# Optimization experiments

Measured on AMD Instinct MI355X. Metric: run time of the kernel, lower is better.

Reference implementation:

```python
import jax, jax.numpy as jnp
import numpy as np

N_NODES = 50000
N_EDGES = 640000
IN_CH, HID, OUT_CH = 128, 256, 3


def setup_inputs() -> dict:
    key = jax.random.key(0)
    ks = jax.random.split(key, 6)
    x = jax.random.normal(ks[0], (N_NODES, IN_CH), dtype=jnp.float32)
    edge_index = jax.random.randint(ks[1], (2, N_EDGES), 0, N_NODES, dtype=jnp.int64)
    # Glorot-ish scaling for weights
    Wl0 = jax.random.normal(ks[2], (IN_CH, HID), dtype=jnp.float32) / np.sqrt(IN_CH)
    bl0 = jnp.zeros((HID,), dtype=jnp.float32)
    Wr0 = jax.random.normal(ks[3], (IN_CH, HID), dtype=jnp.float32) / np.sqrt(IN_CH)
    Wl1 = jax.random.normal(ks[4], (HID, OUT_CH), dtype=jnp.float32) / np.sqrt(HID)
    bl1 = jnp.zeros((OUT_CH,), dtype=jnp.float32)
    Wr1 = jax.random.normal(ks[5], (HID, OUT_CH), dtype=jnp.float32) / np.sqrt(HID)
    return {"x": x, "edge_index": edge_index, "Wl0": Wl0, "bl0": bl0, "Wr0": Wr0,
            "Wl1": Wl1, "bl1": bl1, "Wr1": Wr1}


def _sage_conv(x, src, dst, Wl, bl, Wr, num_nodes):
    # mean aggregation of source features into destination nodes
    msg_sum = jax.ops.segment_sum(x[src], dst, num_segments=num_nodes)  # [N, d_in]
    deg = jax.ops.segment_sum(jnp.ones((src.shape[0],), x.dtype), dst, num_segments=num_nodes)
    mean = msg_sum / jnp.maximum(deg, 1.0)[:, None]
    # PyG SAGEConv: lin_l(aggr) + lin_r(x_self); lin_l carries the bias
    return mean @ Wl + bl + x @ Wr


def reference(x, edge_index, Wl0, bl0, Wr0, Wl1, bl1, Wr1):
    src, dst = edge_index[0], edge_index[1]
    h = _sage_conv(x, src, dst, Wl0, bl0, Wr0, N_NODES)
    h = jax.nn.relu(h)
    # dropout is identity in eval mode (training=False)
    return _sage_conv(h, src, dst, Wl1, bl1, Wr1, N_NODES)
```

## Files before the change

### kernel.cpp

```cpp
#include <hip/hip_runtime.h>

#define NN 50000
#define NNP 50048
#define NE 640000
#define IC 128
#define HC 256
#define OC 3
#define PAD 64

#define TOBF16_BLOCKS (NN * IC / 8 / 256)
#define WPACK_BLOCKS  32
#define DEGZ_BLOCKS   ((NN * 16 / 4 + 255) / 256)

typedef __attribute__((ext_vector_type(8))) short short8;
typedef __attribute__((ext_vector_type(4))) float f32x4;

__device__ __forceinline__ unsigned short f2bf(float f) {
    unsigned int u = __float_as_uint(f);
    unsigned int r = u + 0x7FFFu + ((u >> 16) & 1u);
    return (unsigned short)(r >> 16);
}
__device__ __forceinline__ float bflo(unsigned int v) { return __uint_as_float(v << 16); }
__device__ __forceinline__ float bfhi(unsigned int v) { return __uint_as_float(v & 0xffff0000u); }

__global__ __launch_bounds__(256) void k_prep(const float* __restrict__ x,
                                              const float* __restrict__ Wl0,
                                              const float* __restrict__ Wr0,
                                              unsigned short* __restrict__ Ab,
                                              unsigned short* __restrict__ Bp,
                                              int* __restrict__ degi) {
    int b = blockIdx.x;
    int t = threadIdx.x;
    if (b < TOBF16_BLOCKS) {
        int i = b * 256 + t;
        int n = i >> 4;
        int c = (i & 15) * 8;
        float4 v0 = ((const float4*)x)[i * 2];
        float4 v1 = ((const float4*)x)[i * 2 + 1];
        ushort4 o0, o1;
        o0.x = f2bf(v0.x); o0.y = f2bf(v0.y); o0.z = f2bf(v0.z); o0.w = f2bf(v0.w);
        o1.x = f2bf(v1.x); o1.y = f2bf(v1.y); o1.z = f2bf(v1.z); o1.w = f2bf(v1.w);
        *(ushort4*)&Ab[(size_t)n * 256 + 128 + c] = o0;
        *(ushort4*)&Ab[(size_t)n * 256 + 128 + c + 4] = o1;
    } else if (b < TOBF16_BLOCKS + WPACK_BLOCKS) {
        int tt = (b - TOBF16_BLOCKS) * 256 + t;
        int l = tt & 63;
        int nt = (tt >> 6) & 15;
        int kt = tt >> 10;
        int n = nt * 16 + (l & 15);
        int kbase = kt * 32 + (l >> 4) * 8;
        unsigned short o[8];
        #pragma unroll
        for (int e = 0; e < 8; ++e) {
            int k = kbase + e;
            float w = (k < IC) ? Wl0[k * HC + n] : Wr0[(k - IC) * HC + n];
            o[e] = f2bf(w);
        }
        #pragma unroll
        for (int e = 0; e < 8; ++e) Bp[(size_t)tt * 8 + e] = o[e];
    } else {
        int idx = (b - TOBF16_BLOCKS - WPACK_BLOCKS) * 256 + t;
        if (idx < NN * 16 / 4) ((uint4*)degi)[idx] = make_uint4(0u, 0u, 0u, 0u);
    }
}

__global__ __launch_bounds__(256) void k_build(const int* __restrict__ ei,
                                               int* __restrict__ degi,
                                               unsigned short* __restrict__ csrp) {
    int e = blockIdx.x * blockDim.x + threadIdx.x;
    if (e >= NE) return;
    int src = ei[e];
    int dst = ei[NE + e];
    int rank = atomicAdd(&degi[dst << 4], 1);
    if (rank < PAD) csrp[dst * PAD + rank] = (unsigned short)src;
}

__global__ __launch_bounds__(256) void k_agg(const int* __restrict__ degi,
                                             const unsigned short* __restrict__ csrp,
                                             unsigned short* __restrict__ Ab) {
    int wid = (blockIdx.x * blockDim.x + threadIdx.x) >> 6;
    int lane = threadIdx.x & 63;
    if (wid >= NN) return;
    int deg = min(degi[wid << 4], PAD);
    int beg = wid * PAD;
    int sg = lane >> 3;
    int s  = lane & 7;
    const uint4* base = (const uint4*)Ab;

    float a[16];
    #pragma unroll
    for (int i = 0; i < 16; ++i) a[i] = 0.f;

    for (int j = sg; j < deg; j += 8) {
        int src = csrp[beg + j];
        uint4 v0 = base[(size_t)src * 32 + 16 + s];
        uint4 v1 = base[(size_t)src * 32 + 24 + s];
        a[0] += bflo(v0.x); a[1] += bfhi(v0.x);
        a[2] += bflo(v0.y); a[3] += bfhi(v0.y);
        a[4] += bflo(v0.z); a[5] += bfhi(v0.z);
        a[6] += bflo(v0.w); a[7] += bfhi(v0.w);
        a[8]  += bflo(v1.x); a[9]  += bfhi(v1.x);
        a[10] += bflo(v1.y); a[11] += bfhi(v1.y);
        a[12] += bflo(v1.z); a[13] += bfhi(v1.z);
        a[14] += bflo(v1.w); a[15] += bfhi(v1.w);
    }
    #pragma unroll
    for (int m = 8; m <= 32; m <<= 1)
        #pragma unroll
        for (int i = 0; i < 16; ++i) a[i] += __shfl_xor(a[i], m);

    if (sg == 0) {
        float inv = 1.0f / fmaxf((float)deg, 1.0f);
        uint4 o0, o1;
        o0.x = ((unsigned int)f2bf(a[1] * inv) << 16) | f2bf(a[0] * inv);
        o0.y = ((unsigned int)f2bf(a[3] * inv) << 16) | f2bf(a[2] * inv);
        o0.z = ((unsigned int)f2bf(a[5] * inv) << 16) | f2bf(a[4] * inv);
        o0.w = ((unsigned int)f2bf(a[7] * inv) << 16) | f2bf(a[6] * inv);
        o1.x = ((unsigned int)f2bf(a[9]  * inv) << 16) | f2bf(a[8]  * inv);
        o1.y = ((unsigned int)f2bf(a[11] * inv) << 16) | f2bf(a[10] * inv);
        o1.z = ((unsigned int)f2bf(a[13] * inv) << 16) | f2bf(a[12] * inv);
        o1.w = ((unsigned int)f2bf(a[15] * inv) << 16) | f2bf(a[14] * inv);
        ((uint4*)Ab)[(size_t)wid * 32 + s] = o0;
        ((uint4*)Ab)[(size_t)wid * 32 + 8 + s] = o1;
    }
}

__global__ __launch_bounds__(256, 4) void k_gemm(const unsigned short* __restrict__ Ab,
                                                 const unsigned short* __restrict__ Bp,
                                                 const float* __restrict__ bl0,
                                                 const float* __restrict__ Wl1,
                                                 const float* __restrict__ Wr1,
                                                 float* __restrict__ g,
                                                 float* __restrict__ r) {
    __shared__ float4 Bs[2048];
    __shared__ float wl1s[HC][3];
    __shared__ float wr1s[HC][3];
    __shared__ float bls[HC];

    int t = threadIdx.x;
    for (int i = t; i < HC * 3; i += 256) {
        wl1s[i / 3][i % 3] = Wl1[i];
        wr1s[i / 3][i % 3] = Wr1[i];
    }
    for (int i = t; i < HC; i += 256) bls[i] = bl0[i];

    int w = t >> 6, l = t & 63;
    int n0 = blockIdx.x * 64 + w * 16;

    f32x4 acc[16];
    #pragma unroll
    for (int i = 0; i < 16; ++i) acc[i] = (f32x4){0.f, 0.f, 0.f, 0.f};

    const short8* A8 = (const short8*)Ab + ((size_t)(n0 + (l & 15)) * 32 + (l >> 4));

    for (int q = 0; q < 4; ++q) {
        short8 af0 = A8[(q * 2 + 0) * 4];
        short8 af1 = A8[(q * 2 + 1) * 4];
        __syncthreads();
        const float4* gsrc = (const float4*)(Bp + (size_t)q * 16384) + (w * 64 + l);
        float4* lbase = Bs + w * 64;
        #pragma unroll
        for (int i = 0; i < 8; ++i) {
            __builtin_amdgcn_global_load_lds(
                (const __attribute__((address_space(1))) void*)(gsrc + i * 256),
                (__attribute__((address_space(3))) void*)(lbase + i * 256),
                16, 0, 0);
        }
        __syncthreads();
        const short8* B8 = (const short8*)Bs + l;
        #pragma unroll
        for (int nt = 0; nt < 16; ++nt) {
            short8 bf = B8[nt * 64];
            acc[nt] = __builtin_amdgcn_mfma_f32_16x16x32_bf16(af0, bf, acc[nt], 0, 0, 0);
        }
        B8 = (const short8*)Bs + (1024 + l);
        #pragma unroll
        for (int nt = 0; nt < 16; ++nt) {
            short8 bf = B8[nt * 64];
            acc[nt] = __builtin_amdgcn_mfma_f32_16x16x32_bf16(af1, bf, acc[nt], 0, 0, 0);
        }
    }

    float pl[4][3] = {{0.f}}, pr[4][3] = {{0.f}};
    #pragma unroll
    for (int nt = 0; nt < 16; ++nt) {
        int col = nt * 16 + (l & 15);
        float b = bls[col];
        #pragma unroll
        for (int e = 0; e < 4; ++e) {
            float h = fmaxf(acc[nt][e] + b, 0.0f);
            #pragma unroll
            for (int j = 0; j < 3; ++j) {
                pl[e][j] = fmaf(h, wl1s[col][j], pl[e][j]);
                pr[e][j] = fmaf(h, wr1s[col][j], pr[e][j]);
            }
        }
    }
    #pragma unroll
    for (int m = 1; m <= 8; m <<= 1) {
        #pragma unroll
        for (int e = 0; e < 4; ++e)
            #pragma unroll
            for (int j = 0; j < 3; ++j) {
                pl[e][j] += __shfl_xor(pl[e][j], m);
                pr[e][j] += __shfl_xor(pr[e][j], m);
            }
    }
    if ((l & 15) == 0) {
        #pragma unroll
        for (int e = 0; e < 4; ++e) {
            int node = n0 + (l >> 4) * 4 + e;
            if (node < NN) {
                #pragma unroll
                for (int j = 0; j < 3; ++j) {
                    g[node * 3 + j] = pl[e][j];
                    r[node * 3 + j] = pr[e][j];
                }
            }
        }
    }
}

__global__ __launch_bounds__(256) void k_out(const int* __restrict__ degi,
                                             const unsigned short* __restrict__ csrp,
                                             const float* __restrict__ g,
                                             const float* __restrict__ r,
                                             const float* __restrict__ bl1,
                                             float* __restrict__ out) {
    int tid = blockIdx.x * 256 + threadIdx.x;
    int n = tid >> 3;
    int sl = tid & 7;
    if (n >= NN) return;
    int deg = min(degi[n << 4], PAD);
    int beg = n * PAD;
    float s0 = 0.f, s1 = 0.f, s2 = 0.f;
    for (int j = sl; j < deg; j += 8) {
        int src = csrp[beg + j];
        s0 += g[src * 3 + 0];
        s1 += g[src * 3 + 1];
        s2 += g[src * 3 + 2];
    }
    #pragma unroll
    for (int m = 1; m < 8; m <<= 1) {
        s0 += __shfl_xor(s0, m);
        s1 += __shfl_xor(s1, m);
        s2 += __shfl_xor(s2, m);
    }
    if (sl == 0) {
        float inv = 1.0f / fmaxf((float)deg, 1.0f);
        out[n * 3 + 0] = s0 * inv + bl1[0] + r[n * 3 + 0];
        out[n * 3 + 1] = s1 * inv + bl1[1] + r[n * 3 + 1];
        out[n * 3 + 2] = s2 * inv + bl1[2] + r[n * 3 + 2];
    }
}

extern "C" void kernel_launch(void* const* d_in, const int* in_sizes, int n_in,
                              void* d_out, int out_size, void* d_ws, size_t ws_size,
                              hipStream_t stream) {
    const float* x   = (const float*)d_in[0];
    const int*   ei  = (const int*)d_in[1];
    const float* Wl0 = (const float*)d_in[2];
    const float* bl0 = (const float*)d_in[3];
    const float* Wr0 = (const float*)d_in[4];
    const float* Wl1 = (const float*)d_in[5];
    const float* bl1 = (const float*)d_in[6];
    const float* Wr1 = (const float*)d_in[7];
    float* out = (float*)d_out;

    char* ws = (char*)d_ws;
    int*            degi = (int*)(ws);
    unsigned short* csrp = (unsigned short*)(ws + 3200064);
    unsigned short* Ab   = (unsigned short*)(ws + 9600064);
    unsigned short* Bp   = (unsigned short*)(ws + 35224640);
    float*          g    = (float*)(ws + 35355712);
    float*          r    = (float*)(ws + 35955776);

    k_prep <<<TOBF16_BLOCKS + WPACK_BLOCKS + DEGZ_BLOCKS, 256, 0, stream>>>(x, Wl0, Wr0, Ab, Bp, degi);
    k_build<<<(NE + 255) / 256, 256, 0, stream>>>(ei, degi, csrp);
    k_agg  <<<(NN * 64 + 255) / 256, 256, 0, stream>>>(degi, csrp, Ab);
    k_gemm <<<(NN + 63) / 64, 256, 0, stream>>>(Ab, Bp, bl0, Wl1, Wr1, g, r);
    k_out  <<<(NN * 8 + 255) / 256, 256, 0, stream>>>(degi, csrp, g, r, bl1, out);
}
```

Before: 105.3 us.

## Fuse neighbor aggregation into GEMM via LDS means and merge build with prep

The mean-aggregation kernel is merged into the GEMM kernel. Each block aggregates its 64 nodes into a shared-memory bf16 tile and feeds it directly to the MFMA loop, so the aggregated means no longer round-trip through global memory. The edge-bucketing pass is folded into the bf16 conversion and weight-packing kernel, with degree zeroing split out into its own small kernel. In exchange, the per-block aggregation is serialized before the GEMM and launch bounds drop to 3 waves, which lowers occupancy. The B tile is also now loaded with plain LDS stores instead of global_load_lds.

```diff
diff --git a/kernel.cpp b/kernel.cpp
--- a/kernel.cpp
+++ b/kernel.cpp
@@ -5,12 +5,12 @@
 #define NE 640000
 #define IC 128
 #define HC 256
-#define OC 3
 #define PAD 64
 
+#define BUILD_BLOCKS  ((NE + 255) / 256)
 #define TOBF16_BLOCKS (NN * IC / 8 / 256)
 #define WPACK_BLOCKS  32
-#define DEGZ_BLOCKS   ((NN * 16 / 4 + 255) / 256)
+#define BP_BLOCKS     (BUILD_BLOCKS + TOBF16_BLOCKS + WPACK_BLOCKS)
 
 typedef __attribute__((ext_vector_type(8))) short short8;
 typedef __attribute__((ext_vector_type(4))) float f32x4;
@@ -23,16 +23,31 @@
 __device__ __forceinline__ float bflo(unsigned int v) { return __uint_as_float(v << 16); }
 __device__ __forceinline__ float bfhi(unsigned int v) { return __uint_as_float(v & 0xffff0000u); }
 
-__global__ __launch_bounds__(256) void k_prep(const float* __restrict__ x,
-                                              const float* __restrict__ Wl0,
-                                              const float* __restrict__ Wr0,
-                                              unsigned short* __restrict__ Ab,
-                                              unsigned short* __restrict__ Bp,
-                                              int* __restrict__ degi) {
+__global__ __launch_bounds__(256) void k_zero(int* __restrict__ degi) {
+    int i = blockIdx.x * 256 + threadIdx.x;
+    if (i < NN * 4) ((uint4*)degi)[i] = make_uint4(0u, 0u, 0u, 0u);
+}
+
+__global__ __launch_bounds__(256) void k_bprep(const int* __restrict__ ei,
+                                               const float* __restrict__ x,
+                                               const float* __restrict__ Wl0,
+                                               const float* __restrict__ Wr0,
+                                               int* __restrict__ degi,
+                                               unsigned short* __restrict__ csrp,
+                                               unsigned short* __restrict__ Ax,
+                                               unsigned short* __restrict__ Bp) {
     int b = blockIdx.x;
     int t = threadIdx.x;
-    if (b < TOBF16_BLOCKS) {
-        int i = b * 256 + t;
+    if (b < BUILD_BLOCKS) {
+        int e = b * 256 + t;
+        if (e < NE) {
+            int src = ei[e];
+            int dst = ei[NE + e];
+            int rank = atomicAdd(&degi[dst << 4], 1);
+            if (rank < PAD) csrp[dst * PAD + rank] = (unsigned short)src;
+        }
+    } else if (b < BUILD_BLOCKS + TOBF16_BLOCKS) {
+        int i = (b - BUILD_BLOCKS) * 256 + t;
         int n = i >> 4;
         int c = (i & 15) * 8;
         float4 v0 = ((const float4*)x)[i * 2];
@@ -40,10 +55,10 @@
         ushort4 o0, o1;
         o0.x = f2bf(v0.x); o0.y = f2bf(v0.y); o0.z = f2bf(v0.z); o0.w = f2bf(v0.w);
         o1.x = f2bf(v1.x); o1.y = f2bf(v1.y); o1.z = f2bf(v1.z); o1.w = f2bf(v1.w);
-        *(ushort4*)&Ab[(size_t)n * 256 + 128 + c] = o0;
-        *(ushort4*)&Ab[(size_t)n * 256 + 128 + c + 4] = o1;
-    } else if (b < TOBF16_BLOCKS + WPACK_BLOCKS) {
-        int tt = (b - TOBF16_BLOCKS) * 256 + t;
+        *(ushort4*)&Ax[(size_t)n * 128 + c] = o0;
+        *(ushort4*)&Ax[(size_t)n * 128 + c + 4] = o1;
+    } else {
+        int tt = (b - BUILD_BLOCKS - TOBF16_BLOCKS) * 256 + t;
         int l = tt & 63;
         int nt = (tt >> 6) & 15;
         int kt = tt >> 10;
@@ -58,114 +73,91 @@
         }
         #pragma unroll
         for (int e = 0; e < 8; ++e) Bp[(size_t)tt * 8 + e] = o[e];
-    } else {
-        int idx = (b - TOBF16_BLOCKS - WPACK_BLOCKS) * 256 + t;
-        if (idx < NN * 16 / 4) ((uint4*)degi)[idx] = make_uint4(0u, 0u, 0u, 0u);
-    }
-}
-
-__global__ __launch_bounds__(256) void k_build(const int* __restrict__ ei,
-                                               int* __restrict__ degi,
-                                               unsigned short* __restrict__ csrp) {
-    int e = blockIdx.x * blockDim.x + threadIdx.x;
-    if (e >= NE) return;
-    int src = ei[e];
-    int dst = ei[NE + e];
-    int rank = atomicAdd(&degi[dst << 4], 1);
-    if (rank < PAD) csrp[dst * PAD + rank] = (unsigned short)src;
-}
-
-__global__ __launch_bounds__(256) void k_agg(const int* __restrict__ degi,
-                                             const unsigned short* __restrict__ csrp,
-                                             unsigned short* __restrict__ Ab) {
-    int wid = (blockIdx.x * blockDim.x + threadIdx.x) >> 6;
-    int lane = threadIdx.x & 63;
-    if (wid >= NN) return;
-    int deg = min(degi[wid << 4], PAD);
-    int beg = wid * PAD;
-    int sg = lane >> 3;
-    int s  = lane & 7;
-    const uint4* base = (const uint4*)Ab;
-
-    float a[16];
-    #pragma unroll
-    for (int i = 0; i < 16; ++i) a[i] = 0.f;
-
-    for (int j = sg; j < deg; j += 8) {
-        int src = csrp[beg + j];
-        uint4 v0 = base[(size_t)src * 32 + 16 + s];
-        uint4 v1 = base[(size_t)src * 32 + 24 + s];
-        a[0] += bflo(v0.x); a[1] += bfhi(v0.x);
-        a[2] += bflo(v0.y); a[3] += bfhi(v0.y);
-        a[4] += bflo(v0.z); a[5] += bfhi(v0.z);
-        a[6] += bflo(v0.w); a[7] += bfhi(v0.w);
-        a[8]  += bflo(v1.x); a[9]  += bfhi(v1.x);
-        a[10] += bflo(v1.y); a[11] += bfhi(v1.y);
-        a[12] += bflo(v1.z); a[13] += bfhi(v1.z);
-        a[14] += bflo(v1.w); a[15] += bfhi(v1.w);
-    }
-    #pragma unroll
-    for (int m = 8; m <= 32; m <<= 1)
-        #pragma unroll
-        for (int i = 0; i < 16; ++i) a[i] += __shfl_xor(a[i], m);
-
-    if (sg == 0) {
-        float inv = 1.0f / fmaxf((float)deg, 1.0f);
-        uint4 o0, o1;
-        o0.x = ((unsigned int)f2bf(a[1] * inv) << 16) | f2bf(a[0] * inv);
-        o0.y = ((unsigned int)f2bf(a[3] * inv) << 16) | f2bf(a[2] * inv);
-        o0.z = ((unsigned int)f2bf(a[5] * inv) << 16) | f2bf(a[4] * inv);
-        o0.w = ((unsigned int)f2bf(a[7] * inv) << 16) | f2bf(a[6] * inv);
-        o1.x = ((unsigned int)f2bf(a[9]  * inv) << 16) | f2bf(a[8]  * inv);
-        o1.y = ((unsigned int)f2bf(a[11] * inv) << 16) | f2bf(a[10] * inv);
-        o1.z = ((unsigned int)f2bf(a[13] * inv) << 16) | f2bf(a[12] * inv);
-        o1.w = ((unsigned int)f2bf(a[15] * inv) << 16) | f2bf(a[14] * inv);
-        ((uint4*)Ab)[(size_t)wid * 32 + s] = o0;
-        ((uint4*)Ab)[(size_t)wid * 32 + 8 + s] = o1;
-    }
-}
-
-__global__ __launch_bounds__(256, 4) void k_gemm(const unsigned short* __restrict__ Ab,
-                                                 const unsigned short* __restrict__ Bp,
-                                                 const float* __restrict__ bl0,
-                                                 const float* __restrict__ Wl1,
-                                                 const float* __restrict__ Wr1,
-                                                 float* __restrict__ g,
-                                                 float* __restrict__ r) {
+    }
+}
+
+__global__ __launch_bounds__(256, 3) void k_aggemm(const int* __restrict__ degi,
+                                                   const unsigned short* __restrict__ csrp,
+                                                   const unsigned short* __restrict__ Ax,
+                                                   const unsigned short* __restrict__ Bp,
+                                                   const float* __restrict__ bl0,
+                                                   const float* __restrict__ Wl1,
+                                                   const float* __restrict__ Wr1,
+                                                   float* __restrict__ g,
+                                                   float* __restrict__ r) {
+    __shared__ unsigned short means[64][136];
     __shared__ float4 Bs[2048];
-    __shared__ float wl1s[HC][3];
-    __shared__ float wr1s[HC][3];
-    __shared__ float bls[HC];
-
-    int t = threadIdx.x;
-    for (int i = t; i < HC * 3; i += 256) {
-        wl1s[i / 3][i % 3] = Wl1[i];
-        wr1s[i / 3][i % 3] = Wr1[i];
-    }
-    for (int i = t; i < HC; i += 256) bls[i] = bl0[i];
-
-    int w = t >> 6, l = t & 63;
-    int n0 = blockIdx.x * 64 + w * 16;
+
+    int t = threadIdx.x, w = t >> 6, l = t & 63;
+    int nb = blockIdx.x * 64;
+
+    {
+        int sg = l >> 3;
+        int s  = l & 7;
+        const uint4* base = (const uint4*)Ax;
+        for (int i = 0; i < 16; ++i) {
+            int node = nb + w * 16 + i;
+            int deg = (node < NN) ? min(degi[node << 4], PAD) : 0;
+            int beg = node * PAD;
+            float a[16];
+            #pragma unroll
+            for (int k = 0; k < 16; ++k) a[k] = 0.f;
+            for (int j = sg; j < deg; j += 8) {
+                int src = csrp[beg + j];
+                uint4 v0 = base[(size_t)src * 16 + s];
+                uint4 v1 = base[(size_t)src * 16 + 8 + s];
+                a[0] += bflo(v0.x); a[1] += bfhi(v0.x);
+                a[2] += bflo(v0.y); a[3] += bfhi(v0.y);
+                a[4] += bflo(v0.z); a[5] += bfhi(v0.z);
+                a[6] += bflo(v0.w); a[7] += bfhi(v0.w);
+                a[8]  += bflo(v1.x); a[9]  += bfhi(v1.x);
+                a[10] += bflo(v1.y); a[11] += bfhi(v1.y);
+                a[12] += bflo(v1.z); a[13] += bfhi(v1.z);
+                a[14] += bflo(v1.w); a[15] += bfhi(v1.w);
+            }
+            #pragma unroll
+            for (int m = 8; m <= 32; m <<= 1)
+                #pragma unroll
+                for (int k = 0; k < 16; ++k) a[k] += __shfl_xor(a[k], m);
+            if (sg == 0) {
+                float inv = 1.0f / fmaxf((float)deg, 1.0f);
+                uint4 o0, o1;
+                o0.x = ((unsigned int)f2bf(a[1] * inv) << 16) | f2bf(a[0] * inv);
+                o0.y = ((unsigned int)f2bf(a[3] * inv) << 16) | f2bf(a[2] * inv);
+                o0.z = ((unsigned int)f2bf(a[5] * inv) << 16) | f2bf(a[4] * inv);
+                o0.w = ((unsigned int)f2bf(a[7] * inv) << 16) | f2bf(a[6] * inv);
+                o1.x = ((unsigned int)f2bf(a[9]  * inv) << 16) | f2bf(a[8]  * inv);
+                o1.y = ((unsigned int)f2bf(a[11] * inv) << 16) | f2bf(a[10] * inv);
+                o1.z = ((unsigned int)f2bf(a[13] * inv) << 16) | f2bf(a[12] * inv);
+                o1.w = ((unsigned int)f2bf(a[15] * inv) << 16) | f2bf(a[14] * inv);
+                *(uint4*)&means[w * 16 + i][s * 8] = o0;
+                *(uint4*)&means[w * 16 + i][64 + s * 8] = o1;
+            }
+        }
+    }
+    __syncthreads();
 
     f32x4 acc[16];
     #pragma unroll
     for (int i = 0; i < 16; ++i) acc[i] = (f32x4){0.f, 0.f, 0.f, 0.f};
 
-    const short8* A8 = (const short8*)Ab + ((size_t)(n0 + (l & 15)) * 32 + (l >> 4));
+    const short8* Am  = (const short8*)&means[w * 16 + (l & 15)][(l >> 4) * 8];
+    const short8* A8x = (const short8*)Ax + ((size_t)(nb + w * 16 + (l & 15)) * 16 + (l >> 4));
 
     for (int q = 0; q < 4; ++q) {
-        short8 af0 = A8[(q * 2 + 0) * 4];
-        short8 af1 = A8[(q * 2 + 1) * 4];
+        short8 af0, af1;
+        if (q < 2) {
+            af0 = Am[(q * 2 + 0) * 4];
+            af1 = Am[(q * 2 + 1) * 4];
+        } else {
+            af0 = A8x[(q * 2 - 4) * 4];
+            af1 = A8x[(q * 2 - 3) * 4];
+        }
         __syncthreads();
-        const float4* gsrc = (const float4*)(Bp + (size_t)q * 16384) + (w * 64 + l);
-        float4* lbase = Bs + w * 64;
-        #pragma unroll
-        for (int i = 0; i < 8; ++i) {
-            __builtin_amdgcn_global_load_lds(
-                (const __attribute__((address_space(1))) void*)(gsrc + i * 256),
-                (__attribute__((address_space(3))) void*)(lbase + i * 256),
-                16, 0, 0);
-        }
+        const float4* gsrc = (const float4*)(Bp + (size_t)q * 16384);
+        #pragma unroll
+        for (int i = 0; i < 8; ++i)
+            Bs[i * 256 + t] = gsrc[i * 256 + t];
         __syncthreads();
         const short8* B8 = (const short8*)Bs + l;
         #pragma unroll
@@ -181,18 +173,24 @@
         }
     }
 
+    __syncthreads();
+    float* tb = (float*)Bs;
+    for (int i = t; i < HC * 3; i += 256) { tb[i] = Wl1[i]; tb[768 + i] = Wr1[i]; }
+    tb[1536 + t] = bl0[t];
+    __syncthreads();
+
     float pl[4][3] = {{0.f}}, pr[4][3] = {{0.f}};
     #pragma unroll
     for (int nt = 0; nt < 16; ++nt) {
         int col = nt * 16 + (l & 15);
-        float b = bls[col];
+        float bcol = tb[1536 + col];
         #pragma unroll
         for (int e = 0; e < 4; ++e) {
-            float h = fmaxf(acc[nt][e] + b, 0.0f);
+            float h = fmaxf(acc[nt][e] + bcol, 0.0f);
             #pragma unroll
             for (int j = 0; j < 3; ++j) {
-                pl[e][j] = fmaf(h, wl1s[col][j], pl[e][j]);
-                pr[e][j] = fmaf(h, wr1s[col][j], pr[e][j]);
+                pl[e][j] = fmaf(h, tb[col * 3 + j], pl[e][j]);
+                pr[e][j] = fmaf(h, tb[768 + col * 3 + j], pr[e][j]);
             }
         }
     }
@@ -209,7 +207,7 @@
     if ((l & 15) == 0) {
         #pragma unroll
         for (int e = 0; e < 4; ++e) {
-            int node = n0 + (l >> 4) * 4 + e;
+            int node = nb + w * 16 + (l >> 4) * 4 + e;
             if (node < NN) {
                 #pragma unroll
                 for (int j = 0; j < 3; ++j) {
@@ -270,14 +268,13 @@
     char* ws = (char*)d_ws;
     int*            degi = (int*)(ws);
     unsigned short* csrp = (unsigned short*)(ws + 3200064);
-    unsigned short* Ab   = (unsigned short*)(ws + 9600064);
-    unsigned short* Bp   = (unsigned short*)(ws + 35224640);
-    float*          g    = (float*)(ws + 35355712);
-    float*          r    = (float*)(ws + 35955776);
-
-    k_prep <<<TOBF16_BLOCKS + WPACK_BLOCKS + DEGZ_BLOCKS, 256, 0, stream>>>(x, Wl0, Wr0, Ab, Bp, degi);
-    k_build<<<(NE + 255) / 256, 256, 0, stream>>>(ei, degi, csrp);
-    k_agg  <<<(NN * 64 + 255) / 256, 256, 0, stream>>>(degi, csrp, Ab);
-    k_gemm <<<(NN + 63) / 64, 256, 0, stream>>>(Ab, Bp, bl0, Wl1, Wr1, g, r);
-    k_out  <<<(NN * 8 + 255) / 256, 256, 0, stream>>>(degi, csrp, g, r, bl1, out);
-}
+    unsigned short* Ax   = (unsigned short*)(ws + 9600064);
+    unsigned short* Bp   = (unsigned short*)(ws + 22412352);
+    float*          g    = (float*)(ws + 22543424);
+    float*          r    = (float*)(ws + 23143488);
+
+    k_zero  <<<(NN * 4 + 255) / 256, 256, 0, stream>>>(degi);
+    k_bprep <<<BP_BLOCKS, 256, 0, stream>>>(ei, x, Wl0, Wr0, degi, csrp, Ax, Bp);
+    k_aggemm<<<NNP / 64, 256, 0, stream>>>(degi, csrp, Ax, Bp, bl0, Wl1, Wr1, g, r);
+    k_out   <<<(NN * 8 + 255) / 256, 256, 0, stream>>>(degi, csrp, g, r, bl1, out);
+}
```

Result: slower. 143.5 us (+36.2%).

## Split degree zeroing out and co-schedule edge build with bf16 conversion

Applied to the files above, without the earlier changes.

Zeroing of the degree array moves into its own small kernel. The edge-bucketing (atomic CSR build) is merged into the same launch as the x-to-bf16 conversion and weight packing, so the atomic-bound and bandwidth-bound work can run concurrently on different CUs. The GEMM kernel also replaces the direct global-to-LDS async loads with plain float4 copies through registers. This changes which stages overlap and trades the async LDS load path for a simpler register staging path.

```diff
diff --git a/kernel.cpp b/kernel.cpp
--- a/kernel.cpp
+++ b/kernel.cpp
@@ -5,12 +5,12 @@
 #define NE 640000
 #define IC 128
 #define HC 256
-#define OC 3
 #define PAD 64
 
+#define BUILD_BLOCKS  ((NE + 255) / 256)
 #define TOBF16_BLOCKS (NN * IC / 8 / 256)
 #define WPACK_BLOCKS  32
-#define DEGZ_BLOCKS   ((NN * 16 / 4 + 255) / 256)
+#define BP_BLOCKS     (BUILD_BLOCKS + TOBF16_BLOCKS + WPACK_BLOCKS)
 
 typedef __attribute__((ext_vector_type(8))) short short8;
 typedef __attribute__((ext_vector_type(4))) float f32x4;
@@ -23,16 +23,31 @@
 __device__ __forceinline__ float bflo(unsigned int v) { return __uint_as_float(v << 16); }
 __device__ __forceinline__ float bfhi(unsigned int v) { return __uint_as_float(v & 0xffff0000u); }
 
-__global__ __launch_bounds__(256) void k_prep(const float* __restrict__ x,
-                                              const float* __restrict__ Wl0,
-                                              const float* __restrict__ Wr0,
-                                              unsigned short* __restrict__ Ab,
-                                              unsigned short* __restrict__ Bp,
-                                              int* __restrict__ degi) {
+__global__ __launch_bounds__(256) void k_zero(int* __restrict__ degi) {
+    int i = blockIdx.x * 256 + threadIdx.x;
+    if (i < NN * 4) ((uint4*)degi)[i] = make_uint4(0u, 0u, 0u, 0u);
+}
+
+__global__ __launch_bounds__(256) void k_bprep(const int* __restrict__ ei,
+                                               const float* __restrict__ x,
+                                               const float* __restrict__ Wl0,
+                                               const float* __restrict__ Wr0,
+                                               int* __restrict__ degi,
+                                               unsigned short* __restrict__ csrp,
+                                               unsigned short* __restrict__ Ab,
+                                               unsigned short* __restrict__ Bp) {
     int b = blockIdx.x;
     int t = threadIdx.x;
-    if (b < TOBF16_BLOCKS) {
-        int i = b * 256 + t;
+    if (b < BUILD_BLOCKS) {
+        int e = b * 256 + t;
+        if (e < NE) {
+            int src = ei[e];
+            int dst = ei[NE + e];
+            int rank = atomicAdd(&degi[dst << 4], 1);
+            if (rank < PAD) csrp[dst * PAD + rank] = (unsigned short)src;
+        }
+    } else if (b < BUILD_BLOCKS + TOBF16_BLOCKS) {
+        int i = (b - BUILD_BLOCKS) * 256 + t;
         int n = i >> 4;
         int c = (i & 15) * 8;
         float4 v0 = ((const float4*)x)[i * 2];
@@ -42,8 +57,8 @@
         o1.x = f2bf(v1.x); o1.y = f2bf(v1.y); o1.z = f2bf(v1.z); o1.w = f2bf(v1.w);
         *(ushort4*)&Ab[(size_t)n * 256 + 128 + c] = o0;
         *(ushort4*)&Ab[(size_t)n * 256 + 128 + c + 4] = o1;
-    } else if (b < TOBF16_BLOCKS + WPACK_BLOCKS) {
-        int tt = (b - TOBF16_BLOCKS) * 256 + t;
+    } else {
+        int tt = (b - BUILD_BLOCKS - TOBF16_BLOCKS) * 256 + t;
         int l = tt & 63;
         int nt = (tt >> 6) & 15;
         int kt = tt >> 10;
@@ -58,21 +73,7 @@
         }
         #pragma unroll
         for (int e = 0; e < 8; ++e) Bp[(size_t)tt * 8 + e] = o[e];
-    } else {
-        int idx = (b - TOBF16_BLOCKS - WPACK_BLOCKS) * 256 + t;
-        if (idx < NN * 16 / 4) ((uint4*)degi)[idx] = make_uint4(0u, 0u, 0u, 0u);
-    }
-}
-
-__global__ __launch_bounds__(256) void k_build(const int* __restrict__ ei,
-                                               int* __restrict__ degi,
-                                               unsigned short* __restrict__ csrp) {
-    int e = blockIdx.x * blockDim.x + threadIdx.x;
-    if (e >= NE) return;
-    int src = ei[e];
-    int dst = ei[NE + e];
-    int rank = atomicAdd(&degi[dst << 4], 1);
-    if (rank < PAD) csrp[dst * PAD + rank] = (unsigned short)src;
+    }
 }
 
 __global__ __launch_bounds__(256) void k_agg(const int* __restrict__ degi,
@@ -157,15 +158,10 @@
         short8 af0 = A8[(q * 2 + 0) * 4];
         short8 af1 = A8[(q * 2 + 1) * 4];
         __syncthreads();
-        const float4* gsrc = (const float4*)(Bp + (size_t)q * 16384) + (w * 64 + l);
-        float4* lbase = Bs + w * 64;
-        #pragma unroll
-        for (int i = 0; i < 8; ++i) {
-            __builtin_amdgcn_global_load_lds(
-                (const __attribute__((address_space(1))) void*)(gsrc + i * 256),
-                (__attribute__((address_space(3))) void*)(lbase + i * 256),
-                16, 0, 0);
-        }
+        const float4* gsrc = (const float4*)(Bp + (size_t)q * 16384);
+        #pragma unroll
+        for (int i = 0; i < 8; ++i)
+            Bs[i * 256 + t] = gsrc[i * 256 + t];
         __syncthreads();
         const short8* B8 = (const short8*)Bs + l;
         #pragma unroll
@@ -275,8 +271,8 @@
     float*          g    = (float*)(ws + 35355712);
     float*          r    = (float*)(ws + 35955776);
 
-    k_prep <<<TOBF16_BLOCKS + WPACK_BLOCKS + DEGZ_BLOCKS, 256, 0, stream>>>(x, Wl0, Wr0, Ab, Bp, degi);
-    k_build<<<(NE + 255) / 256, 256, 0, stream>>>(ei, degi, csrp);
+    k_zero <<<(NN * 4 + 255) / 256, 256, 0, stream>>>(degi);
+    k_bprep<<<BP_BLOCKS, 256, 0, stream>>>(ei, x, Wl0, Wr0, degi, csrp, Ab, Bp);
     k_agg  <<<(NN * 64 + 255) / 256, 256, 0, stream>>>(degi, csrp, Ab);
     k_gemm <<<(NN + 63) / 64, 256, 0, stream>>>(Ab, Bp, bl0, Wl1, Wr1, g, r);
     k_out  <<<(NN * 8 + 255) / 256, 256, 0, stream>>>(degi, csrp, g, r, bl1, out);
```

New measurement: 108.2 us. 2.7% more time.
